# Kernel tuning notes

Measured on AMD Instinct MI355X. Metric: run time of the kernel, lower is better.

The kernel has to match this reference:

```python
import jax, jax.numpy as jnp
import numpy as np

M, N, K = 4096, 8192, 4096


def setup_inputs() -> dict:
    key = jax.random.key(0)
    k1, k2, k3, k4 = jax.random.split(key, 4)
    a = jax.random.randint(k1, (M, K), 0, 127, dtype=jnp.int32)  # int8 activations
    b = jax.random.randint(k2, (N, K), 0, 127, dtype=jnp.int32)  # int8 weights (row-major [N,K])
    alpha_row = jax.random.uniform(k3, (M, 1), dtype=jnp.float16)  # per-row dequant scale
    alpha_col = jax.random.uniform(k4, (1, N), dtype=jnp.float16)  # per-col dequant scale
    return {"a": a, "b": b, "alpha_row": alpha_row, "alpha_col": alpha_col}


def reference(a, b, alpha_row, alpha_col):
    # x = a @ b.T in fp32 (int8 values upcast), then rescale by outer product of scales
    x = jnp.matmul(a.astype(jnp.float32), b.astype(jnp.float32).T)  # [M, N]
    scale = alpha_row.astype(jnp.float32) * alpha_col.astype(jnp.float32)  # [M, N] via broadcast
    out = x * scale
    return out.astype(jnp.float16)
```

## Files before the change

kernel.cpp:

```cpp
#include <hip/hip_runtime.h>
#include <cstdint>
#include <cstddef>

#define M_DIM 4096
#define N_DIM 8192
#define K_DIM 4096

typedef __attribute__((ext_vector_type(4))) int int4v;

__global__ void __launch_bounds__(256) pack_frag(const int* __restrict__ a,
                                                 const int* __restrict__ b,
                                                 unsigned char* __restrict__ pa,
                                                 unsigned char* __restrict__ pb) {
    size_t t = (size_t)blockIdx.x * 256 + threadIdx.x;
    const size_t NA = (size_t)(M_DIM / 16) * (K_DIM / 64) * 64;
    const int* __restrict__ src;
    unsigned char* __restrict__ dst;
    if (t < NA) {
        src = a; dst = pa;
    } else {
        src = b; dst = pb; t -= NA;
    }
    const int l = (int)(t & 63);
    const int s = (int)((t >> 6) & 63);
    const int p = (int)(t >> 12);
    const int* g = src + ((size_t)(16 * p + (l & 15))) * K_DIM + s * 64 + (l >> 4) * 16;
    const int4v* g4 = (const int4v*)g;
    int4v o;
#pragma unroll
    for (int q = 0; q < 4; ++q) {
        int4v v = g4[q];
        o[q] = (v[0] & 0xff) | ((v[1] & 0xff) << 8) | ((v[2] & 0xff) << 16) | (v[3] << 24);
    }
    ((int4v*)dst)[t] = o;
}

__device__ inline void async_copy16(const unsigned char* g, unsigned char* l) {
    __builtin_amdgcn_global_load_lds(
        (const __attribute__((address_space(1))) void*)g,
        (__attribute__((address_space(3))) void*)l,
        16, 0, 0);
}

__global__ void __launch_bounds__(256, 2) gemm_i8(const unsigned char* __restrict__ Ap,
                                                  const unsigned char* __restrict__ Bp,
                                                  const _Float16* __restrict__ arow,
                                                  const _Float16* __restrict__ acol,
                                                  _Float16* __restrict__ Cout) {
    __shared__ __align__(16) unsigned char As[2 * 8192];
    __shared__ __align__(16) unsigned char Bs[2 * 16384];

    const int tid  = threadIdx.x;
    const int lane = tid & 63;
    const int wave = tid >> 6;
    const int bn   = blockIdx.x;
    const int bm   = blockIdx.y;

    const int pm0 = (wave & 1) * 4;
    const int pn0 = (wave >> 1) * 8;

    const unsigned char* ag[2];
    int salo[2];
#pragma unroll
    for (int r = 0; r < 2; ++r) {
        const int p = 2 * wave + r;
        ag[r]   = Ap + (size_t)(bm * 8 + p) * 65536 + lane * 16;
        salo[r] = p * 1024;
    }
    const unsigned char* bg[4];
    int sblo[4];
#pragma unroll
    for (int r = 0; r < 4; ++r) {
        const int p = 4 * wave + r;
        bg[r]   = Bp + (size_t)(bn * 16 + p) * 65536 + lane * 16;
        sblo[r] = p * 1024;
    }

    const int a_off = pm0 * 1024 + lane * 16;
    const int b_off = pn0 * 1024 + lane * 16;

    int4v acc[4][8];
#pragma unroll
    for (int i = 0; i < 4; ++i)
#pragma unroll
        for (int j = 0; j < 8; ++j) acc[i][j] = (int4v)0;

    const int NT = K_DIM / 64;

#pragma unroll
    for (int r = 0; r < 2; ++r) async_copy16(ag[r], As + salo[r]);
#pragma unroll
    for (int r = 0; r < 4; ++r) async_copy16(bg[r], Bs + sblo[r]);
    __syncthreads();

#pragma unroll 2
    for (int T = 0; T < NT; ++T) {
        const int ca = (T & 1) * 8192;
        const int cb = (T & 1) * 16384;

        if (T + 1 < NT) {
            const size_t gko = (size_t)(T + 1) * 1024;
#pragma unroll
            for (int r = 0; r < 2; ++r)
                async_copy16(ag[r] + gko, As + (ca ^ 8192) + salo[r]);
#pragma unroll
            for (int r = 0; r < 4; ++r)
                async_copy16(bg[r] + gko, Bs + (cb ^ 16384) + sblo[r]);
        }

        int4v af[4], bf[8];
#pragma unroll
        for (int i = 0; i < 4; ++i)
            af[i] = *(const int4v*)(As + ca + a_off + i * 1024);
#pragma unroll
        for (int j = 0; j < 8; ++j)
            bf[j] = *(const int4v*)(Bs + cb + b_off + j * 1024);

#pragma unroll
        for (int i = 0; i < 4; ++i)
#pragma unroll
            for (int j = 0; j < 8; ++j)
                acc[i][j] = __builtin_amdgcn_mfma_i32_16x16x64_i8(af[i], bf[j],
                                                                  acc[i][j], 0, 0, 0);

        __syncthreads();
    }

    const int gcol0 = bn * 256 + pn0 * 16 + (lane & 15);
    float ac8[8];
#pragma unroll
    for (int j = 0; j < 8; ++j) ac8[j] = (float)acol[gcol0 + j * 16];

    const size_t grow0 = (size_t)bm * 128 + pm0 * 16 + (lane >> 4) * 4;
#pragma unroll
    for (int i = 0; i < 4; ++i) {
#pragma unroll
        for (int r = 0; r < 4; ++r) {
            const size_t row = grow0 + i * 16 + r;
            const float ar = (float)arow[row];
            _Float16* outp = Cout + row * (size_t)N_DIM + gcol0;
#pragma unroll
            for (int j = 0; j < 8; ++j) {
                float v = (float)acc[i][j][r] * ar * ac8[j];
                outp[j * 16] = (_Float16)v;
            }
        }
    }
}

extern "C" void kernel_launch(void* const* d_in, const int* in_sizes, int n_in,
                              void* d_out, int out_size, void* d_ws, size_t ws_size,
                              hipStream_t stream) {
    const int* a = (const int*)d_in[0];
    const int* b = (const int*)d_in[1];
    const _Float16* ar = (const _Float16*)d_in[2];
    const _Float16* ac = (const _Float16*)d_in[3];
    _Float16* out = (_Float16*)d_out;

    unsigned char* pa = (unsigned char*)d_ws;
    unsigned char* pb = pa + (size_t)M_DIM * K_DIM;

    const size_t total_frag = (size_t)(M_DIM / 16 + N_DIM / 16) * (K_DIM / 64) * 64;
    pack_frag<<<(int)(total_frag / 256), 256, 0, stream>>>(a, b, pa, pb);

    dim3 grid(N_DIM / 256, M_DIM / 128);
    gemm_i8<<<grid, 256, 0, stream>>>(pa, pb, ar, ac, out);
}
```

Before: 371.4 us.

## Enlarge GEMM tile to 256x256 with 8 waves and triple-buffered ping-pong pipeline

New measurement: 381.0 us. 1.03x slower.

```diff
diff --git a/kernel.cpp b/kernel.cpp
--- a/kernel.cpp
+++ b/kernel.cpp
@@ -42,106 +42,156 @@
         16, 0, 0);
 }
 
-__global__ void __launch_bounds__(256, 2) gemm_i8(const unsigned char* __restrict__ Ap,
+#define BAR() __builtin_amdgcn_s_barrier()
+#define WAIT_LGKM0() asm volatile("s_waitcnt lgkmcnt(0)" ::: "memory")
+
+__global__ void __launch_bounds__(512, 2) gemm_i8(const unsigned char* __restrict__ Ap,
                                                   const unsigned char* __restrict__ Bp,
                                                   const _Float16* __restrict__ arow,
                                                   const _Float16* __restrict__ acol,
                                                   _Float16* __restrict__ Cout) {
-    __shared__ __align__(16) unsigned char As[2 * 8192];
-    __shared__ __align__(16) unsigned char Bs[2 * 16384];
+    __shared__ __align__(16) unsigned char lds[3 * 32768];
 
     const int tid  = threadIdx.x;
     const int lane = tid & 63;
     const int wave = tid >> 6;
+    const int wr   = wave >> 2;
+    const int wc   = wave & 3;
     const int bn   = blockIdx.x;
     const int bm   = blockIdx.y;
 
-    const int pm0 = (wave & 1) * 4;
-    const int pn0 = (wave >> 1) * 8;
-
-    const unsigned char* ag[2];
-    int salo[2];
+    const unsigned char* aG[2];
+    const unsigned char* bG[2];
+    int aL[2], bL[2];
 #pragma unroll
     for (int r = 0; r < 2; ++r) {
         const int p = 2 * wave + r;
-        ag[r]   = Ap + (size_t)(bm * 8 + p) * 65536 + lane * 16;
-        salo[r] = p * 1024;
-    }
-    const unsigned char* bg[4];
-    int sblo[4];
-#pragma unroll
-    for (int r = 0; r < 4; ++r) {
-        const int p = 4 * wave + r;
-        bg[r]   = Bp + (size_t)(bn * 16 + p) * 65536 + lane * 16;
-        sblo[r] = p * 1024;
-    }
-
-    const int a_off = pm0 * 1024 + lane * 16;
-    const int b_off = pn0 * 1024 + lane * 16;
-
-    int4v acc[4][8];
-#pragma unroll
-    for (int i = 0; i < 4; ++i)
-#pragma unroll
-        for (int j = 0; j < 8; ++j) acc[i][j] = (int4v)0;
+        aG[r] = Ap + (size_t)(bm * 16 + p) * 65536 + lane * 16;
+        aL[r] = p * 1024;
+        bG[r] = Bp + (size_t)(bn * 16 + p) * 65536 + lane * 16;
+        bL[r] = 16384 + p * 1024;
+    }
+
+    const int a_off = wr * 8192 + lane * 16;
+    const int b_off = 16384 + wc * 4096 + lane * 16;
+
+    int4v acc[8][4];
+#pragma unroll
+    for (int i = 0; i < 8; ++i)
+#pragma unroll
+        for (int j = 0; j < 4; ++j) acc[i][j] = (int4v)0;
 
     const int NT = K_DIM / 64;
 
 #pragma unroll
-    for (int r = 0; r < 2; ++r) async_copy16(ag[r], As + salo[r]);
-#pragma unroll
-    for (int r = 0; r < 4; ++r) async_copy16(bg[r], Bs + sblo[r]);
-    __syncthreads();
-
-#pragma unroll 2
+    for (int t = 0; t < 2; ++t) {
+        const size_t gk = (size_t)t * 1024;
+        const int lo = t * 32768;
+        async_copy16(aG[0] + gk, lds + lo + aL[0]);
+        async_copy16(aG[1] + gk, lds + lo + aL[1]);
+        async_copy16(bG[0] + gk, lds + lo + bL[0]);
+        async_copy16(bG[1] + gk, lds + lo + bL[1]);
+    }
+    asm volatile("s_waitcnt vmcnt(4)" ::: "memory");
+    BAR();
+
+    int o_cur = 0, o_nxt = 32768, o_pre = 65536;
+
     for (int T = 0; T < NT; ++T) {
-        const int ca = (T & 1) * 8192;
-        const int cb = (T & 1) * 16384;
-
-        if (T + 1 < NT) {
-            const size_t gko = (size_t)(T + 1) * 1024;
-#pragma unroll
-            for (int r = 0; r < 2; ++r)
-                async_copy16(ag[r] + gko, As + (ca ^ 8192) + salo[r]);
-#pragma unroll
-            for (int r = 0; r < 4; ++r)
-                async_copy16(bg[r] + gko, Bs + (cb ^ 16384) + sblo[r]);
+        const bool pre = (T + 2 < NT);
+        const size_t gk2 = (size_t)(T + 2) * 1024;
+        const unsigned char* Ac = lds + o_cur;
+
+        int4v af[4], bf01[2], bf23[2];
+
+#pragma unroll
+        for (int i = 0; i < 4; ++i)
+            af[i] = *(const int4v*)(Ac + a_off + i * 1024);
+#pragma unroll
+        for (int j = 0; j < 2; ++j)
+            bf01[j] = *(const int4v*)(Ac + b_off + j * 1024);
+        if (pre) async_copy16(aG[0] + gk2, lds + o_pre + aL[0]);
+        BAR();
+        WAIT_LGKM0();
+        __builtin_amdgcn_s_setprio(1);
+#pragma unroll
+        for (int i = 0; i < 4; ++i)
+#pragma unroll
+            for (int j = 0; j < 2; ++j)
+                acc[i][j] = __builtin_amdgcn_mfma_i32_16x16x64_i8(af[i], bf01[j],
+                                                                  acc[i][j], 0, 0, 0);
+        __builtin_amdgcn_s_setprio(0);
+        BAR();
+
+#pragma unroll
+        for (int j = 0; j < 2; ++j)
+            bf23[j] = *(const int4v*)(Ac + b_off + (2 + j) * 1024);
+        if (pre) async_copy16(aG[1] + gk2, lds + o_pre + aL[1]);
+        BAR();
+        WAIT_LGKM0();
+        __builtin_amdgcn_s_setprio(1);
+#pragma unroll
+        for (int i = 0; i < 4; ++i)
+#pragma unroll
+            for (int j = 0; j < 2; ++j)
+                acc[i][2 + j] = __builtin_amdgcn_mfma_i32_16x16x64_i8(af[i], bf23[j],
+                                                                      acc[i][2 + j], 0, 0, 0);
+        __builtin_amdgcn_s_setprio(0);
+        BAR();
+
+#pragma unroll
+        for (int i = 0; i < 4; ++i)
+            af[i] = *(const int4v*)(Ac + a_off + (4 + i) * 1024);
+        if (pre) async_copy16(bG[0] + gk2, lds + o_pre + bL[0]);
+        BAR();
+        WAIT_LGKM0();
+        __builtin_amdgcn_s_setprio(1);
+#pragma unroll
+        for (int i = 0; i < 4; ++i)
+#pragma unroll
+            for (int j = 0; j < 2; ++j)
+                acc[4 + i][2 + j] = __builtin_amdgcn_mfma_i32_16x16x64_i8(af[i], bf23[j],
+                                                                          acc[4 + i][2 + j], 0, 0, 0);
+        __builtin_amdgcn_s_setprio(0);
+        BAR();
+
+        if (pre) async_copy16(bG[1] + gk2, lds + o_pre + bL[1]);
+        BAR();
+        __builtin_amdgcn_s_setprio(1);
+#pragma unroll
+        for (int i = 0; i < 4; ++i)
+#pragma unroll
+            for (int j = 0; j < 2; ++j)
+                acc[4 + i][j] = __builtin_amdgcn_mfma_i32_16x16x64_i8(af[i], bf01[j],
+                                                                      acc[4 + i][j], 0, 0, 0);
+        __builtin_amdgcn_s_setprio(0);
+
+        if (pre) {
+            asm volatile("s_waitcnt vmcnt(4)" ::: "memory");
+        } else {
+            asm volatile("s_waitcnt vmcnt(0)" ::: "memory");
         }
-
-        int4v af[4], bf[8];
-#pragma unroll
-        for (int i = 0; i < 4; ++i)
-            af[i] = *(const int4v*)(As + ca + a_off + i * 1024);
-#pragma unroll
-        for (int j = 0; j < 8; ++j)
-            bf[j] = *(const int4v*)(Bs + cb + b_off + j * 1024);
-
-#pragma unroll
-        for (int i = 0; i < 4; ++i)
-#pragma unroll
-            for (int j = 0; j < 8; ++j)
-                acc[i][j] = __builtin_amdgcn_mfma_i32_16x16x64_i8(af[i], bf[j],
-                                                                  acc[i][j], 0, 0, 0);
-
-        __syncthreads();
-    }
-
-    const int gcol0 = bn * 256 + pn0 * 16 + (lane & 15);
-    float ac8[8];
-#pragma unroll
-    for (int j = 0; j < 8; ++j) ac8[j] = (float)acol[gcol0 + j * 16];
-
-    const size_t grow0 = (size_t)bm * 128 + pm0 * 16 + (lane >> 4) * 4;
-#pragma unroll
-    for (int i = 0; i < 4; ++i) {
+        BAR();
+
+        const int t0 = o_cur; o_cur = o_nxt; o_nxt = o_pre; o_pre = t0;
+    }
+
+    const int gcol0 = bn * 256 + wc * 64 + (lane & 15);
+    float ac4[4];
+#pragma unroll
+    for (int j = 0; j < 4; ++j) ac4[j] = (float)acol[gcol0 + j * 16];
+
+    const size_t grow0 = (size_t)bm * 256 + wr * 128 + (lane >> 4) * 4;
+#pragma unroll
+    for (int i = 0; i < 8; ++i) {
 #pragma unroll
         for (int r = 0; r < 4; ++r) {
             const size_t row = grow0 + i * 16 + r;
             const float ar = (float)arow[row];
             _Float16* outp = Cout + row * (size_t)N_DIM + gcol0;
 #pragma unroll
-            for (int j = 0; j < 8; ++j) {
-                float v = (float)acc[i][j][r] * ar * ac8[j];
+            for (int j = 0; j < 4; ++j) {
+                float v = (float)acc[i][j][r] * ar * ac4[j];
                 outp[j * 16] = (_Float16)v;
             }
         }
@@ -163,6 +213,6 @@
     const size_t total_frag = (size_t)(M_DIM / 16 + N_DIM / 16) * (K_DIM / 64) * 64;
     pack_frag<<<(int)(total_frag / 256), 256, 0, stream>>>(a, b, pa, pb);
 
-    dim3 grid(N_DIM / 256, M_DIM / 128);
-    gemm_i8<<<grid, 256, 0, stream>>>(pa, pb, ar, ac, out);
-}
+    dim3 grid(N_DIM / 256, M_DIM / 256);
+    gemm_i8<<<grid, 512, 0, stream>>>(pa, pb, ar, ac, out);
+}
```

## Triple-buffer LDS with prefetch distance two and partial vmcnt waits

Applied to the files above, without the earlier changes.

After: 359.2 us. 3.3% less time.

```diff
diff --git a/kernel.cpp b/kernel.cpp
--- a/kernel.cpp
+++ b/kernel.cpp
@@ -42,13 +42,14 @@
         16, 0, 0);
 }
 
+#define BAR() __builtin_amdgcn_s_barrier()
+
 __global__ void __launch_bounds__(256, 2) gemm_i8(const unsigned char* __restrict__ Ap,
                                                   const unsigned char* __restrict__ Bp,
                                                   const _Float16* __restrict__ arow,
                                                   const _Float16* __restrict__ acol,
                                                   _Float16* __restrict__ Cout) {
-    __shared__ __align__(16) unsigned char As[2 * 8192];
-    __shared__ __align__(16) unsigned char Bs[2 * 16384];
+    __shared__ __align__(16) unsigned char lds[3 * 24576];
 
     const int tid  = threadIdx.x;
     const int lane = tid & 63;
@@ -73,11 +74,11 @@
     for (int r = 0; r < 4; ++r) {
         const int p = 4 * wave + r;
         bg[r]   = Bp + (size_t)(bn * 16 + p) * 65536 + lane * 16;
-        sblo[r] = p * 1024;
+        sblo[r] = 8192 + p * 1024;
     }
 
     const int a_off = pm0 * 1024 + lane * 16;
-    const int b_off = pn0 * 1024 + lane * 16;
+    const int b_off = 8192 + pn0 * 1024 + lane * 16;
 
     int4v acc[4][8];
 #pragma unroll
@@ -88,42 +89,59 @@
     const int NT = K_DIM / 64;
 
 #pragma unroll
-    for (int r = 0; r < 2; ++r) async_copy16(ag[r], As + salo[r]);
+    for (int t = 0; t < 2; ++t) {
+        const size_t gk = (size_t)t * 1024;
+        const int lo = t * 24576;
 #pragma unroll
-    for (int r = 0; r < 4; ++r) async_copy16(bg[r], Bs + sblo[r]);
-    __syncthreads();
+        for (int r = 0; r < 2; ++r) async_copy16(ag[r] + gk, lds + lo + salo[r]);
+#pragma unroll
+        for (int r = 0; r < 4; ++r) async_copy16(bg[r] + gk, lds + lo + sblo[r]);
+    }
+    asm volatile("s_waitcnt vmcnt(6)" ::: "memory");
+    BAR();
 
-#pragma unroll 2
+    int o_cur = 0, o_nxt = 24576, o_pre = 49152;
+
+#pragma unroll 3
     for (int T = 0; T < NT; ++T) {
-        const int ca = (T & 1) * 8192;
-        const int cb = (T & 1) * 16384;
+        const bool pre = (T + 2 < NT);
+        const unsigned char* Ac = lds + o_cur;
 
-        if (T + 1 < NT) {
-            const size_t gko = (size_t)(T + 1) * 1024;
+        if (pre) {
+            const size_t gk2 = (size_t)(T + 2) * 1024;
 #pragma unroll
             for (int r = 0; r < 2; ++r)
-                async_copy16(ag[r] + gko, As + (ca ^ 8192) + salo[r]);
+                async_copy16(ag[r] + gk2, lds + o_pre + salo[r]);
 #pragma unroll
             for (int r = 0; r < 4; ++r)
-                async_copy16(bg[r] + gko, Bs + (cb ^ 16384) + sblo[r]);
+                async_copy16(bg[r] + gk2, lds + o_pre + sblo[r]);
         }
 
         int4v af[4], bf[8];
 #pragma unroll
         for (int i = 0; i < 4; ++i)
-            af[i] = *(const int4v*)(As + ca + a_off + i * 1024);
+            af[i] = *(const int4v*)(Ac + a_off + i * 1024);
 #pragma unroll
         for (int j = 0; j < 8; ++j)
-            bf[j] = *(const int4v*)(Bs + cb + b_off + j * 1024);
+            bf[j] = *(const int4v*)(Ac + b_off + j * 1024);
 
+        __builtin_amdgcn_s_setprio(1);
 #pragma unroll
         for (int i = 0; i < 4; ++i)
 #pragma unroll
             for (int j = 0; j < 8; ++j)
                 acc[i][j] = __builtin_amdgcn_mfma_i32_16x16x64_i8(af[i], bf[j],
                                                                   acc[i][j], 0, 0, 0);
+        __builtin_amdgcn_s_setprio(0);
 
-        __syncthreads();
+        if (pre) {
+            asm volatile("s_waitcnt vmcnt(6)" ::: "memory");
+        } else {
+            asm volatile("s_waitcnt vmcnt(0)" ::: "memory");
+        }
+        BAR();
+
+        const int t0 = o_cur; o_cur = o_nxt; o_nxt = o_pre; o_pre = t0;
     }
 
     const int gcol0 = bn * 256 + pn0 * 16 + (lane & 15);
```
